# Performance work log

Measured on AMD Instinct MI355X. Metric: run time of the kernel, lower is better.

The kernel has to match this reference:

```python
import jax, jax.numpy as jnp
import numpy as np

PATCH = 16  # pooling patch size used by the surrogate feature extractor


def setup_inputs() -> dict:
    key = jax.random.key(0)
    k1, k2, k3, k4 = jax.random.split(key, 4)
    B, C, H, W = 8, 3, 224, 224
    S = 196        # max_segments
    D = 768        # embed_dim
    P = H // PATCH # 14
    feat_in = C * P * P  # 588
    img = jax.random.normal(k1, (B, C, H, W), dtype=jnp.float32)
    seg_logits = jax.random.normal(k2, (B, S, H, W), dtype=jnp.float32)
    w_proj = jax.random.normal(k3, (feat_in, D), dtype=jnp.float32) * 0.02
    b_proj = jax.random.normal(k4, (D,), dtype=jnp.float32) * 0.02
    return {"img": img, "seg_logits": seg_logits, "w_proj": w_proj, "b_proj": b_proj}


def reference(img, seg_logits, w_proj, b_proj):
    B, C, H, W = img.shape
    S = seg_logits.shape[1]
    K = PATCH
    P, Q = H // K, W // K

    # per-pixel hard segment labels (torch.max over channel dim)
    labels = jnp.argmax(seg_logits, axis=1)                      # [B,H,W] int
    mask = jax.nn.one_hot(labels, S, dtype=img.dtype)            # [B,H,W,S]
    maskr = mask.transpose(0, 3, 1, 2).reshape(B, S, P, K, Q, K)  # [B,S,P,K,Q,K]
    imgr = img.reshape(B, C, P, K, Q, K)                          # [B,C,P,K,Q,K]

    # segmented_image = image * segment_mask, patch-mean-pooled, done for all
    # segments at once without materializing [B,S,C,H,W]
    pooled = jnp.einsum('bspkql,bcpkql->bscpq', maskr, imgr) / (K * K)  # [B,S,C,P,Q]
    feat = pooled.reshape(B, S, -1) @ w_proj + b_proj             # [B,S,D]

    # compact features of PRESENT segments contiguously (sorted by label,
    # matching torch.unique ordering), absent segments dropped
    pix_count = jnp.sum(maskr, axis=(2, 3, 4, 5))                 # [B,S]
    present = pix_count > 0                                       # [B,S]
    pos = jnp.cumsum(present.astype(jnp.int32), axis=1) - 1       # [B,S]
    pos_safe = jnp.where(present, pos, S)                         # S -> dropped

    out = jnp.zeros((B, S, feat.shape[-1]), dtype=img.dtype)
    out = out.at[jnp.arange(B)[:, None], pos_safe].set(feat, mode='drop')
    return out
```

## Files before the change

### kernel.cpp

```cpp
#include <hip/hip_runtime.h>

#define BB   8
#define CC   3
#define HH   224
#define WW   224
#define SS   196
#define DD   768
#define PP   14
#define QQ   14
#define HWSZ (HH * WW)
#define KIN  (CC * PP * QQ)
#define PQ   (PP * QQ)

__global__ __launch_bounds__(256) void k_argmax_pool(
    const float* __restrict__ seg, const float* __restrict__ img,
    float* __restrict__ pooled, int* __restrict__ presence)
{
    int t  = blockIdx.x * 256 + threadIdx.x;
    int b  = t / (HWSZ / 4);
    int f4 = t - b * (HWSZ / 4);
    int f  = f4 * 4;

    const float4* sp = (const float4*)(seg + (long)b * SS * HWSZ + f);
    const int str4 = HWSZ / 4;

    float4 m = sp[0];
    int lx = 0, ly = 0, lz = 0, lw = 0;
    #pragma unroll 8
    for (int s = 1; s < SS; ++s) {
        float4 v = sp[(size_t)s * str4];
        if (v.x > m.x) { m.x = v.x; lx = s; }
        if (v.y > m.y) { m.y = v.y; ly = s; }
        if (v.z > m.z) { m.z = v.z; lz = s; }
        if (v.w > m.w) { m.w = v.w; lw = s; }
    }

    float4 i0 = *(const float4*)(img + ((long)(b * CC + 0)) * HWSZ + f);
    float4 i1 = *(const float4*)(img + ((long)(b * CC + 1)) * HWSZ + f);
    float4 i2 = *(const float4*)(img + ((long)(b * CC + 2)) * HWSZ + f);

    int   labs[4]  = { lx, ly, lz, lw };
    float imv[4][3] = { { i0.x, i1.x, i2.x }, { i0.y, i1.y, i2.y },
                        { i0.z, i1.z, i2.z }, { i0.w, i1.w, i2.w } };

    #pragma unroll
    for (int j = 0; j < 4; ++j) {
        int ff  = f + j;
        int h   = ff / WW;
        int w   = ff - h * WW;
        int p   = h >> 4;
        int q   = w >> 4;
        int lab = labs[j];
        long pb = (long)(b * SS + lab) * KIN + p * QQ + q;
        atomicAdd(&pooled[pb],          imv[j][0] * (1.0f / 256.0f));
        atomicAdd(&pooled[pb + PQ],     imv[j][1] * (1.0f / 256.0f));
        atomicAdd(&pooled[pb + 2 * PQ], imv[j][2] * (1.0f / 256.0f));
        presence[b * SS + lab] = 1;
    }
}

__global__ __launch_bounds__(256) void k_pos(
    const int* __restrict__ presence, int* __restrict__ pos)
{
    int b = blockIdx.x;
    int s = threadIdx.x;
    __shared__ int sc[256];

    int pres = (s < SS) ? (presence[b * SS + s] != 0 ? 1 : 0) : 0;
    sc[s] = pres;
    __syncthreads();

    for (int off = 1; off < 256; off <<= 1) {
        int v = (s >= off) ? sc[s - off] : 0;
        __syncthreads();
        sc[s] += v;
        __syncthreads();
    }
    if (s < SS) pos[b * SS + s] = pres ? (sc[s] - 1) : -1;
}

__global__ __launch_bounds__(256) void k_gemm(
    const float* __restrict__ pooled, const float* __restrict__ wp,
    const float* __restrict__ bp, const int* __restrict__ pos,
    float* __restrict__ out)
{
    int row0 = blockIdx.x * 8;
    int d    = threadIdx.x + blockIdx.y * 256;

    const float* A = pooled + (long)row0 * KIN;

    float acc[8] = {0.f, 0.f, 0.f, 0.f, 0.f, 0.f, 0.f, 0.f};

    #pragma unroll 2
    for (int k4 = 0; k4 < KIN / 4; ++k4) {
        int kb = k4 * 4;
        float w0 = wp[(long)(kb + 0) * DD + d];
        float w1 = wp[(long)(kb + 1) * DD + d];
        float w2 = wp[(long)(kb + 2) * DD + d];
        float w3 = wp[(long)(kb + 3) * DD + d];
        #pragma unroll
        for (int r = 0; r < 8; ++r) {
            float4 a = *(const float4*)(A + (long)r * KIN + kb);
            acc[r] += a.x * w0;
            acc[r] += a.y * w1;
            acc[r] += a.z * w2;
            acc[r] += a.w * w3;
        }
    }

    float bias = bp[d];
    #pragma unroll
    for (int r = 0; r < 8; ++r) {
        int row = row0 + r;
        int p   = pos[row];
        if (p >= 0) {
            int b = row / SS;
            out[((long)(b * SS + p)) * DD + d] = acc[r] + bias;
        }
    }
}

extern "C" void kernel_launch(void* const* d_in, const int* in_sizes, int n_in,
                              void* d_out, int out_size, void* d_ws, size_t ws_size,
                              hipStream_t stream) {
    const float* img  = (const float*)d_in[0];
    const float* seg  = (const float*)d_in[1];
    const float* wp   = (const float*)d_in[2];
    const float* bp   = (const float*)d_in[3];
    float* out = (float*)d_out;

    const size_t pooled_bytes   = (size_t)BB * SS * KIN * sizeof(float);
    const size_t presence_bytes = (size_t)BB * SS * sizeof(int);
    float* pooled   = (float*)d_ws;
    int*   presence = (int*)((char*)d_ws + pooled_bytes);
    int*   pos      = (int*)((char*)d_ws + pooled_bytes + presence_bytes);

    hipMemsetAsync(d_ws, 0, pooled_bytes + presence_bytes, stream);
    hipMemsetAsync(d_out, 0, (size_t)out_size * sizeof(float), stream);

    {
        int total_threads = BB * HWSZ / 4;
        dim3 grid(total_threads / 256);
        k_argmax_pool<<<grid, 256, 0, stream>>>(seg, img, pooled, presence);
    }

    k_pos<<<dim3(BB), 256, 0, stream>>>(presence, pos);

    {
        dim3 grid(SS * BB / 8, DD / 256);
        k_gemm<<<grid, 256, 0, stream>>>(pooled, wp, bp, pos, out);
    }
}
```

Measured before the change: 544.1 us.

## Pool patches in shared memory and write per-patch presence instead of global atomics

```diff
diff --git a/kernel.cpp b/kernel.cpp
--- a/kernel.cpp
+++ b/kernel.cpp
@@ -12,14 +12,27 @@
 #define KIN  (CC * PP * QQ)
 #define PQ   (PP * QQ)
 
-__global__ __launch_bounds__(256) void k_argmax_pool(
+__global__ __launch_bounds__(128) void k_argmax_pool(
     const float* __restrict__ seg, const float* __restrict__ img,
-    float* __restrict__ pooled, int* __restrict__ presence)
+    float* __restrict__ pooled, int* __restrict__ pres2)
 {
-    int t  = blockIdx.x * 256 + threadIdx.x;
-    int b  = t / (HWSZ / 4);
-    int f4 = t - b * (HWSZ / 4);
-    int f  = f4 * 4;
+    const int b   = blockIdx.y;
+    const int p   = blockIdx.x / 7;
+    const int q0  = (blockIdx.x % 7) * 2;
+    const int tid = threadIdx.x;
+    const int r   = tid >> 3;
+    const int c4  = tid & 7;
+    const int pat = c4 >> 2;
+
+    const int h = p * 16 + r;
+    const int w = q0 * 16 + c4 * 4;
+    const int f = h * WW + w;
+
+    __shared__ float accf[2 * SS * 3];
+    __shared__ int   flag[2 * SS];
+    for (int i = tid; i < 2 * SS * 3; i += 128) accf[i] = 0.f;
+    for (int i = tid; i < 2 * SS;     i += 128) flag[i] = 0;
+    __syncthreads();
 
     const float4* sp = (const float4*)(seg + (long)b * SS * HWSZ + f);
     const int str4 = HWSZ / 4;
@@ -39,34 +52,50 @@
     float4 i1 = *(const float4*)(img + ((long)(b * CC + 1)) * HWSZ + f);
     float4 i2 = *(const float4*)(img + ((long)(b * CC + 2)) * HWSZ + f);
 
-    int   labs[4]  = { lx, ly, lz, lw };
+    int   labs[4]   = { lx, ly, lz, lw };
     float imv[4][3] = { { i0.x, i1.x, i2.x }, { i0.y, i1.y, i2.y },
                         { i0.z, i1.z, i2.z }, { i0.w, i1.w, i2.w } };
 
+    float* accp = accf + pat * SS * 3;
+    int*   flp  = flag + pat * SS;
     #pragma unroll
     for (int j = 0; j < 4; ++j) {
-        int ff  = f + j;
-        int h   = ff / WW;
-        int w   = ff - h * WW;
-        int p   = h >> 4;
-        int q   = w >> 4;
         int lab = labs[j];
-        long pb = (long)(b * SS + lab) * KIN + p * QQ + q;
-        atomicAdd(&pooled[pb],          imv[j][0] * (1.0f / 256.0f));
-        atomicAdd(&pooled[pb + PQ],     imv[j][1] * (1.0f / 256.0f));
-        atomicAdd(&pooled[pb + 2 * PQ], imv[j][2] * (1.0f / 256.0f));
-        presence[b * SS + lab] = 1;
+        atomicAdd(&accp[lab * 3 + 0], imv[j][0]);
+        atomicAdd(&accp[lab * 3 + 1], imv[j][1]);
+        atomicAdd(&accp[lab * 3 + 2], imv[j][2]);
+        flp[lab] = 1;
+    }
+    __syncthreads();
+
+    for (int ss = tid; ss < 2 * SS; ss += 128) {
+        int pt = ss >= SS;
+        int s  = ss - pt * SS;
+        int q  = q0 + pt;
+        long base = (long)(b * SS + s) * KIN + p * QQ + q;
+        const float* a = accf + (pt * SS + s) * 3;
+        pooled[base]          = a[0] * (1.0f / 256.0f);
+        pooled[base + PQ]     = a[1] * (1.0f / 256.0f);
+        pooled[base + 2 * PQ] = a[2] * (1.0f / 256.0f);
+        pres2[((long)b * PQ + p * QQ + q) * SS + s] = flag[pt * SS + s];
     }
 }
 
 __global__ __launch_bounds__(256) void k_pos(
-    const int* __restrict__ presence, int* __restrict__ pos)
+    const int* __restrict__ pres2, int* __restrict__ pos)
 {
     int b = blockIdx.x;
     int s = threadIdx.x;
+
+    int pres = 0;
+    if (s < SS) {
+        const int* pp = pres2 + (long)b * PQ * SS + s;
+        #pragma unroll 4
+        for (int pq = 0; pq < PQ; ++pq) pres |= pp[(long)pq * SS];
+    }
+    pres = pres ? 1 : 0;
+
     __shared__ int sc[256];
-
-    int pres = (s < SS) ? (presence[b * SS + s] != 0 ? 1 : 0) : 0;
     sc[s] = pres;
     __syncthreads();
 
@@ -129,22 +158,20 @@
     const float* bp   = (const float*)d_in[3];
     float* out = (float*)d_out;
 
-    const size_t pooled_bytes   = (size_t)BB * SS * KIN * sizeof(float);
-    const size_t presence_bytes = (size_t)BB * SS * sizeof(int);
-    float* pooled   = (float*)d_ws;
-    int*   presence = (int*)((char*)d_ws + pooled_bytes);
-    int*   pos      = (int*)((char*)d_ws + pooled_bytes + presence_bytes);
+    const size_t pooled_bytes = (size_t)BB * SS * KIN * sizeof(float);
+    const size_t pres2_bytes  = (size_t)BB * PQ * SS * sizeof(int);
+    float* pooled = (float*)d_ws;
+    int*   pres2  = (int*)((char*)d_ws + pooled_bytes);
+    int*   pos    = (int*)((char*)d_ws + pooled_bytes + pres2_bytes);
 
-    hipMemsetAsync(d_ws, 0, pooled_bytes + presence_bytes, stream);
     hipMemsetAsync(d_out, 0, (size_t)out_size * sizeof(float), stream);
 
     {
-        int total_threads = BB * HWSZ / 4;
-        dim3 grid(total_threads / 256);
-        k_argmax_pool<<<grid, 256, 0, stream>>>(seg, img, pooled, presence);
+        dim3 grid(PP * 7, BB);
+        k_argmax_pool<<<grid, 128, 0, stream>>>(seg, img, pooled, pres2);
     }
 
-    k_pos<<<dim3(BB), 256, 0, stream>>>(presence, pos);
+    k_pos<<<dim3(BB), 256, 0, stream>>>(pres2, pos);
 
     {
         dim3 grid(SS * BB / 8, DD / 256);
```

New measurement: 532.3 us. 2.2% less time.
